# Optimization experiments

Measured on AMD Instinct MI355X. Metric: run time of the kernel, lower is better.

## Reference

```python
import jax, jax.numpy as jnp
import numpy as np

ALPHA = 0.5  # trapezoidal_alpha

def rmsnorm(x, w, eps=1e-5):
    return x * jax.lax.rsqrt(jnp.mean(x * x, axis=-1, keepdims=True) + eps) * w

def ssd_scan(x, Bc, Cc, dt, A, alpha):
    # x: (B,L,H,P), Bc/Cc: (B,L,N), dt: (B,L,H), A: (H,)
    da = jnp.exp(dt * A)  # (B,L,H), A < 0 so da in (0,1)
    shift = lambda t: jnp.concatenate([jnp.zeros_like(t[:, :1]), t[:, :-1]], axis=1)
    xp, bp, dtp = shift(x), shift(Bc), shift(dt)
    to_t = lambda t: jnp.moveaxis(t, 1, 0)
    xs = tuple(map(to_t, (x, Bc, Cc, dt, da, xp, bp, dtp)))
    Bb, _, H, P = x.shape
    N = Bc.shape[-1]
    h0 = jnp.zeros((Bb, H, P, N), x.dtype)
    def step(h, inp):
        xt, bt, ct, dtt, dat, xpt, bpt, dtpt = inp
        u = dtt[:, :, None, None] * xt[..., None] * bt[:, None, None, :]      # (B,H,P,N)
        up = dtpt[:, :, None, None] * xpt[..., None] * bpt[:, None, None, :]  # prev input term
        h = dat[:, :, None, None] * (h + alpha * up) + (1.0 - alpha) * u      # trapezoidal update
        y = jnp.einsum('bhpn,bn->bhp', h, ct)
        return h, y
    _, ys = jax.lax.scan(step, h0, xs)
    return jnp.moveaxis(ys, 0, 1)  # (B,L,H,P)

def setup_inputs() -> dict:
    key = jax.random.key(0)
    ks = jax.random.split(key, 10)
    B, NV, NQ = 4, 256, 32
    D, DI, H, N, E, NL = 1024, 2048, 32, 128, 1536, 12
    PROJ = 2 * DI + 2 * N + H  # z | x | B | C | dt
    s = 0.02
    return {
        'visual_tokens': jax.random.normal(ks[0], (B, NV, D), jnp.float32),
        'query_embeds': jax.random.normal(ks[1], (B, NQ, D), jnp.float32),
        'vis_w': jax.random.normal(ks[2], (D, D), jnp.float32) * s,
        'vis_b': jnp.zeros((D,), jnp.float32),
        'qry_w': jax.random.normal(ks[3], (D, D), jnp.float32) * s,
        'qry_b': jnp.zeros((D,), jnp.float32),
        'norm_ws': jnp.ones((NL, D), jnp.float32),
        'in_ws': jax.random.normal(ks[4], (NL, D, PROJ), jnp.float32) * s,
        'dt_biases': jax.random.normal(ks[5], (NL, H), jnp.float32) * 0.5,
        'A_logs': jnp.log(jnp.tile(jnp.arange(1.0, H + 1.0, dtype=jnp.float32)[None], (NL, 1))),
        'D_ssm': jnp.ones((NL, H), jnp.float32),
        'gnorm_ws': jnp.ones((NL, DI), jnp.float32),
        'out_ws': jax.random.normal(ks[6], (NL, DI, D), jnp.float32) * s,
        'norm_f_w': jnp.ones((D,), jnp.float32),
        'head_w': jax.random.normal(ks[7], (D, E), jnp.float32) * s,
        'head_b': jnp.zeros((E,), jnp.float32),
    }

def reference(visual_tokens, query_embeds, vis_w, vis_b, qry_w, qry_b, norm_ws, in_ws,
              dt_biases, A_logs, D_ssm, gnorm_ws, out_ws, norm_f_w, head_w, head_b):
    vis = visual_tokens @ vis_w + vis_b
    qry = query_embeds @ qry_w + qry_b
    hidden = jnp.concatenate([vis, qry], axis=1)  # (B,L,D)
    n_layers = in_ws.shape[0]
    d_inner = gnorm_ws.shape[-1]
    H = A_logs.shape[-1]
    P = d_inner // H
    N = (in_ws.shape[-1] - 2 * d_inner - H) // 2
    for i in range(n_layers):
        res = hidden
        xin = rmsnorm(hidden, norm_ws[i])
        proj = xin @ in_ws[i]  # (B,L,2*DI+2*N+H)
        z = proj[..., :d_inner]
        xss = proj[..., d_inner:2 * d_inner]
        Bc = proj[..., 2 * d_inner:2 * d_inner + N]
        Cc = proj[..., 2 * d_inner + N:2 * d_inner + 2 * N]
        dt = jax.nn.softplus(proj[..., 2 * d_inner + 2 * N:] + dt_biases[i])
        A = -jnp.exp(A_logs[i])
        xr = xss.reshape(xss.shape[0], xss.shape[1], H, P)
        y = ssd_scan(xr, Bc, Cc, dt, A, ALPHA) + D_ssm[i][None, None, :, None] * xr
        y = y.reshape(xss.shape)
        y = rmsnorm(y * jax.nn.silu(z), gnorm_ws[i])  # gated RMSNorm
        hidden = res + y @ out_ws[i]
    hidden = rmsnorm(hidden, norm_f_w)
    pooled = hidden.mean(axis=1)                   # (B,D)
    out = pooled @ head_w + head_b                 # (B,E)
    nrm = jnp.linalg.norm(out, axis=-1, keepdims=True)
    return out / jnp.maximum(nrm, 1e-12)           # F.normalize semantics
```

## Files before the change

kernel.cpp:

```cpp
#include <hip/hip_runtime.h>
#include <cmath>

#define Bb   4
#define Tt   288
#define Dd   1024
#define DIi  2048
#define HH   32
#define PP   64
#define NNs  128
#define PROJ  4384
#define PROJP 4480
#define NLl  12
#define EE   1536

typedef __bf16 bf16x8 __attribute__((ext_vector_type(8)));
typedef float f32x4 __attribute__((ext_vector_type(4)));
typedef float f32x16 __attribute__((ext_vector_type(16)));

__device__ __forceinline__ unsigned short f2bf(float v) {
  __bf16 b = (__bf16)v;
  return __builtin_bit_cast(unsigned short, b);
}
__device__ __forceinline__ float bf2f(unsigned short u) {
  unsigned int x = ((unsigned int)u) << 16;
  return __builtin_bit_cast(float, x);
}
__device__ __forceinline__ void split2(float v, unsigned short& h, unsigned short& l) {
  h = f2bf(v);
  l = f2bf(v - bf2f(h));
}

__device__ __forceinline__ size_t packed_off(int row, int k, int K) {
  size_t tile = (size_t)(row >> 5) * (K >> 5) + (k >> 5);
  int half = (k >> 4) & 1;
  int lane = (row & 31) + (((k >> 3) & 1) << 5);
  return tile * 1024 + half * 512 + lane * 8 + (k & 7);
}

__device__ __forceinline__ void async16(const void* g, void* l) {
  __builtin_amdgcn_global_load_lds(
      (const __attribute__((address_space(1))) unsigned int*)g,
      (__attribute__((address_space(3))) unsigned int*)l, 16, 0, 0);
}

__device__ inline float block_reduce_sum(float v, float* lds) {
#pragma unroll
  for (int d = 32; d > 0; d >>= 1) v += __shfl_down(v, d, 64);
  int lane = threadIdx.x & 63;
  int w = threadIdx.x >> 6;
  if (lane == 0) lds[w] = v;
  __syncthreads();
  if (threadIdx.x == 0) {
    float s = lds[0];
    int nw = blockDim.x >> 6;
    for (int i = 1; i < nw; i++) s += lds[i];
    lds[0] = s;
  }
  __syncthreads();
  return lds[0];
}

__global__ __launch_bounds__(256) void cvt_act_k(const float* __restrict__ vis,
                                                 const float* __restrict__ qry,
                                                 unsigned short* __restrict__ oh,
                                                 unsigned short* __restrict__ ol) {
  int idx = (blockIdx.x * 256 + threadIdx.x) * 4;
  const float* src = (idx < 1024 * 1024) ? &vis[idx] : &qry[idx - 1024 * 1024];
  float4 v = *(const float4*)src;
  ushort4 h, l;
  split2(v.x, h.x, l.x); split2(v.y, h.y, l.y);
  split2(v.z, h.z, l.z); split2(v.w, h.w, l.w);
  size_t po = packed_off(idx >> 10, idx & 1023, 1024);
  *(ushort4*)&oh[po] = h;
  *(ushort4*)&ol[po] = l;
}

__global__ __launch_bounds__(256) void cvt_tr2_k(const float* __restrict__ W,
                                                 unsigned short* __restrict__ Wth,
                                                 unsigned short* __restrict__ Wtl,
                                                 int K, int N,
                                                 size_t wstride, size_t ostride) {
  __shared__ float tile[32][33];
  W   += (size_t)blockIdx.z * wstride;
  Wth += (size_t)blockIdx.z * ostride;
  Wtl += (size_t)blockIdx.z * ostride;
  const int n0 = blockIdx.x * 32, k0 = blockIdx.y * 32;
  const int c = threadIdx.x & 31;
  const int r0 = threadIdx.x >> 5;
#pragma unroll
  for (int j = 0; j < 4; j++) {
    int r = r0 + j * 8;
    int n = n0 + c;
    tile[r][c] = (n < N) ? W[(size_t)(k0 + r) * N + n] : 0.f;
  }
  __syncthreads();
  const int nl = threadIdx.x >> 3;
  const int kl = (threadIdx.x & 7) * 4;
  ushort4 h, l;
  split2(tile[kl + 0][nl], h.x, l.x);
  split2(tile[kl + 1][nl], h.y, l.y);
  split2(tile[kl + 2][nl], h.z, l.z);
  split2(tile[kl + 3][nl], h.w, l.w);
  size_t o = packed_off(n0 + nl, k0 + kl, K);
  *(ushort4*)&Wth[o] = h;
  *(ushort4*)&Wtl[o] = l;
}

template<int BM, int BN>
__global__ __launch_bounds__(256) void gemm3_k(
    const unsigned short* __restrict__ Ah, const unsigned short* __restrict__ Al,
    const unsigned short* __restrict__ Wh, const unsigned short* __restrict__ Wl,
    const float* __restrict__ bias, const float* __restrict__ res,
    float* __restrict__ C, int M, int N, int K,
    int rows_per_b, int T_total, int t_off)
{
  constexpr int FM = BM / 64;
  constexpr int FN = BN / 64;
  __shared__ __align__(16) unsigned short Ash[BM * 32];
  __shared__ __align__(16) unsigned short Asl[BM * 32];
  __shared__ __align__(16) unsigned short Bsh[BN * 32];
  __shared__ __align__(16) unsigned short Bsl[BN * 32];
  const int tid = threadIdx.x;
  const int lane = tid & 63;
  const int wm = (tid >> 6) >> 1;
  const int wn = (tid >> 6) & 1;
  const int m0 = blockIdx.y * BM;
  const int n0 = blockIdx.x * BN;
  const int lrow = lane & 31;
  const int kb32 = K >> 5;

  f32x16 acc[FM][FN];
#pragma unroll
  for (int i = 0; i < FM; i++)
#pragma unroll
    for (int j = 0; j < FN; j++) acc[i][j] = (f32x16)0.0f;

  for (int kb = 0; kb < kb32; kb++) {
#pragma unroll
    for (int c = 0; c < BM / 64; c++) {
      int o = (c * 256 + tid) * 16;
      int t = o >> 11;
      size_t gb = (((size_t)((m0 >> 5) + t) * kb32 + kb) << 11) + (o & 2047);
      async16((const char*)Ah + gb, (char*)Ash + o);
      async16((const char*)Al + gb, (char*)Asl + o);
    }
#pragma unroll
    for (int c = 0; c < BN / 64; c++) {
      int o = (c * 256 + tid) * 16;
      int t = o >> 11;
      size_t gb = (((size_t)((n0 >> 5) + t) * kb32 + kb) << 11) + (o & 2047);
      async16((const char*)Wh + gb, (char*)Bsh + o);
      async16((const char*)Wl + gb, (char*)Bsl + o);
    }
    __syncthreads();

#pragma unroll
    for (int kh = 0; kh < 2; kh++) {
      bf16x8 ah[FM], al[FM], bh[FN], bl[FN];
#pragma unroll
      for (int i = 0; i < FM; i++) {
        int off = (wm * FM + i) * 1024 + kh * 512 + lane * 8;
        ah[i] = *(const bf16x8*)&Ash[off];
        al[i] = *(const bf16x8*)&Asl[off];
      }
#pragma unroll
      for (int j = 0; j < FN; j++) {
        int off = (wn * FN + j) * 1024 + kh * 512 + lane * 8;
        bh[j] = *(const bf16x8*)&Bsh[off];
        bl[j] = *(const bf16x8*)&Bsl[off];
      }
#pragma unroll
      for (int i = 0; i < FM; i++)
#pragma unroll
        for (int j = 0; j < FN; j++) {
          acc[i][j] = __builtin_amdgcn_mfma_f32_32x32x16_bf16(ah[i], bh[j], acc[i][j], 0, 0, 0);
          acc[i][j] = __builtin_amdgcn_mfma_f32_32x32x16_bf16(ah[i], bl[j], acc[i][j], 0, 0, 0);
          acc[i][j] = __builtin_amdgcn_mfma_f32_32x32x16_bf16(al[i], bh[j], acc[i][j], 0, 0, 0);
        }
    }
    __syncthreads();
  }

  const int r0 = (lane >> 5) * 4;
#pragma unroll
  for (int i = 0; i < FM; i++) {
#pragma unroll
    for (int j = 0; j < FN; j++) {
      int ncol = n0 + wn * (BN / 2) + j * 32 + lrow;
      float bv = bias ? bias[ncol] : 0.f;
#pragma unroll
      for (int rg = 0; rg < 16; rg++) {
        int m = m0 + wm * (BM / 2) + i * 32 + (rg & 3) + 8 * (rg >> 2) + r0;
        size_t orow;
        if (T_total) {
          int bbv = m / rows_per_b;
          orow = (size_t)bbv * T_total + (m - bbv * rows_per_b) + t_off;
        } else {
          orow = (size_t)m;
        }
        float v = acc[i][j][rg] + bv;
        if (res) v += res[orow * N + ncol];
        C[orow * N + ncol] = v;
      }
    }
  }
}

__global__ __launch_bounds__(256) void gemm_k(
    const float* __restrict__ A, const float* __restrict__ W,
    const float* __restrict__ bias, const float* __restrict__ res,
    float* __restrict__ C, int M, int N, int K,
    int rows_per_b, int T_total, int t_off)
{
  __shared__ float As[16][64];
  __shared__ float Ws[16][64];
  const int tid = threadIdx.x;
  const int tx = tid & 15;
  const int ty = tid >> 4;
  const int m0 = blockIdx.y * 64;
  const int n0 = blockIdx.x * 64;
  float acc[4][4] = {};
  const int ar = tid >> 2;
  const int ac = (tid & 3) << 2;
  const int wr = tid >> 4;
  const int wc = (tid & 15) << 2;

  for (int k0 = 0; k0 < K; k0 += 16) {
    float4 av = {0.f, 0.f, 0.f, 0.f};
    int gr = m0 + ar;
    if (gr < M) av = *(const float4*)&A[(size_t)gr * K + k0 + ac];
    As[ac + 0][ar] = av.x; As[ac + 1][ar] = av.y;
    As[ac + 2][ar] = av.z; As[ac + 3][ar] = av.w;

    float4 wv = {0.f, 0.f, 0.f, 0.f};
    int gc = n0 + wc;
    const float* wp = &W[(size_t)(k0 + wr) * N + gc];
    if (gc + 3 < N) {
      wv = *(const float4*)wp;
    } else {
      if (gc + 0 < N) wv.x = wp[0];
      if (gc + 1 < N) wv.y = wp[1];
      if (gc + 2 < N) wv.z = wp[2];
    }
    *(float4*)&Ws[wr][wc] = wv;
    __syncthreads();
#pragma unroll
    for (int kk = 0; kk < 16; kk++) {
      float4 a4 = *(const float4*)&As[kk][ty << 2];
      float4 b4 = *(const float4*)&Ws[kk][tx << 2];
      float a[4] = {a4.x, a4.y, a4.z, a4.w};
      float b[4] = {b4.x, b4.y, b4.z, b4.w};
#pragma unroll
      for (int i = 0; i < 4; i++)
#pragma unroll
        for (int j = 0; j < 4; j++)
          acc[i][j] = fmaf(a[i], b[j], acc[i][j]);
    }
    __syncthreads();
  }
#pragma unroll
  for (int i = 0; i < 4; i++) {
    int gr = m0 + (ty << 2) + i;
    if (gr >= M) continue;
    int bbv = gr / rows_per_b;
    int tt = gr - bbv * rows_per_b;
    size_t orow = (size_t)bbv * T_total + tt + t_off;
#pragma unroll
    for (int j = 0; j < 4; j++) {
      int gc = n0 + (tx << 2) + j;
      if (gc >= N) continue;
      float v = acc[i][j];
      if (bias) v += bias[gc];
      if (res)  v += res[orow * (size_t)N + gc];
      C[orow * (size_t)N + gc] = v;
    }
  }
}

__global__ __launch_bounds__(256) void rmsnorm_k(
    const float* __restrict__ x, const float* __restrict__ w, float* __restrict__ out)
{
  __shared__ float lds[8];
  const int row = blockIdx.x;
  const float* xr = x + (size_t)row * Dd;
  float4 v = *(const float4*)&xr[threadIdx.x << 2];
  float ss = v.x * v.x + v.y * v.y + v.z * v.z + v.w * v.w;
  ss = block_reduce_sum(ss, lds);
  float sc = rsqrtf(ss * (1.f / Dd) + 1e-5f);
  float4 wv = *(const float4*)&w[threadIdx.x << 2];
  float4 o = {v.x * sc * wv.x, v.y * sc * wv.y, v.z * sc * wv.z, v.w * sc * wv.w};
  *(float4*)&out[(size_t)row * Dd + (threadIdx.x << 2)] = o;
}

__global__ __launch_bounds__(256) void rmsnorm2_k(
    const float* __restrict__ x, const float* __restrict__ w,
    unsigned short* __restrict__ oh, unsigned short* __restrict__ ol)
{
  __shared__ float lds[8];
  const int row = blockIdx.x;
  const float* xr = x + (size_t)row * Dd;
  float4 v = *(const float4*)&xr[threadIdx.x << 2];
  float ss = v.x * v.x + v.y * v.y + v.z * v.z + v.w * v.w;
  ss = block_reduce_sum(ss, lds);
  float sc = rsqrtf(ss * (1.f / Dd) + 1e-5f);
  float4 wv = *(const float4*)&w[threadIdx.x << 2];
  ushort4 h, l;
  split2(v.x * sc * wv.x, h.x, l.x);
  split2(v.y * sc * wv.y, h.y, l.y);
  split2(v.z * sc * wv.z, h.z, l.z);
  split2(v.w * sc * wv.w, h.w, l.w);
  size_t o = packed_off(row, threadIdx.x << 2, 1024);
  *(ushort4*)&oh[o] = h;
  *(ushort4*)&ol[o] = l;
}

__global__ __launch_bounds__(64) void dtcum_k(
    const float* __restrict__ proj, const float* __restrict__ dt_bias,
    const float* __restrict__ A_log,
    float* __restrict__ dtt, double* __restrict__ dcum)
{
  const int h = blockIdx.x & 31;
  const int b = blockIdx.x >> 5;
  const int lane = threadIdx.x;
  const float A = -expf(A_log[h]);
  const float bias = dt_bias[h];
  const int rowo = (b * HH + h) * Tt;
  double base = 0.0;
  for (int c = 0; c < (Tt + 63) / 64; c++) {
    int t = c * 64 + lane;
    float dt = 0.f;
    if (t < Tt) {
      float v = proj[(size_t)(b * Tt + t) * PROJP + 2 * DIi + 2 * NNs + h] + bias;
      dt = (v > 20.f) ? v : log1pf(expf(v));
    }
    double a = (double)(dt * A);
#pragma unroll
    for (int d = 1; d < 64; d <<= 1) {
      double o = __shfl_up(a, d, 64);
      if (lane >= d) a += o;
    }
    double cum = base + a;
    if (t < Tt) { dtt[rowo + t] = dt; dcum[rowo + t] = cum; }
    base = __shfl(cum, 63, 64);
  }
}

__global__ __launch_bounds__(256) void cbgemm_k(const float* __restrict__ proj,
                                                float* __restrict__ St)
{
  const int tI = blockIdx.x, jI = blockIdx.y, b = blockIdx.z;
  if (jI > tI) return;
  __shared__ float Ct[32][130];
  __shared__ float Bt[32][130];
  const int tid = threadIdx.x;
  const int r = tid >> 3;
  const int q = (tid & 7) * 16;
  const float* pb = proj + (size_t)b * Tt * PROJP;
  {
    const float* crow = pb + (size_t)(tI * 32 + r) * PROJP + 2 * DIi + NNs + q;
    const float* brow = pb + (size_t)(jI * 32 + r) * PROJP + 2 * DIi + q;
#pragma unroll
    for (int f = 0; f < 16; f += 4) {
      float4 c4 = *(const float4*)&crow[f];
      float4 b4 = *(const float4*)&brow[f];
      *(float2*)&Ct[r][q + f]     = make_float2(c4.x, c4.y);
      *(float2*)&Ct[r][q + f + 2] = make_float2(c4.z, c4.w);
      *(float2*)&Bt[r][q + f]     = make_float2(b4.x, b4.y);
      *(float2*)&Bt[r][q + f + 2] = make_float2(b4.z, b4.w);
    }
  }
  __syncthreads();
  const int j_r = tid >> 3;
  const int t_c = (tid & 7) * 4;
  float acc[4] = {0.f, 0.f, 0.f, 0.f};
  for (int n = 0; n < NNs; n += 2) {
    float2 b2 = *(const float2*)&Bt[j_r][n];
#pragma unroll
    for (int k = 0; k < 4; k++) {
      float2 c2 = *(const float2*)&Ct[t_c + k][n];
      acc[k] = fmaf(b2.x, c2.x, acc[k]);
      acc[k] = fmaf(b2.y, c2.y, acc[k]);
    }
  }
  float* so = St + ((size_t)b * Tt + jI * 32 + j_r) * Tt + tI * 32 + t_c;
  *(float4*)so = make_float4(acc[0], acc[1], acc[2], acc[3]);
}

__global__ __launch_bounds__(256) void ssd_y_k(
    const float* __restrict__ proj, const float* __restrict__ St,
    const float* __restrict__ dtt, const double* __restrict__ dcum,
    const float* __restrict__ Dssm, float* __restrict__ ybuf)
{
  const int tI = blockIdx.x;
  const int h  = blockIdx.y;
  const int b  = blockIdx.z;
  __shared__ __align__(16) float Xs[32][64];
  __shared__ __align__(16) float Ss[32][36];
  __shared__ double cjs[32];
  const int tid = threadIdx.x;
  const int t_l = tid & 31;
  const int pg  = tid >> 5;
  const int t0  = tI * 32;
  const int rowo = (b * HH + h) * Tt;
  const double ct = dcum[rowo + t0 + t_l];
  const float Ds = Dssm[h];
  const float* pb = proj + (size_t)b * Tt * PROJP;
  float y[8] = {0,0,0,0,0,0,0,0};
  const int sr = tid >> 3;
  const int sq = tid & 7;

  for (int jI = 0; jI <= tI; jI++) {
    const int j0 = jI * 32;
    {
      const float* xr = pb + (size_t)(j0 + sr) * PROJP + DIi + h * PP + sq * 8;
      *(float4*)&Xs[sr][sq * 8]     = *(const float4*)&xr[0];
      *(float4*)&Xs[sr][sq * 8 + 4] = *(const float4*)&xr[4];
    }
    {
      const float* srow = St + ((size_t)b * Tt + j0 + sr) * Tt + t0 + sq * 4;
      float4 s4 = *(const float4*)srow;
      float dj = dtt[rowo + j0 + sr];
      s4.x *= dj; s4.y *= dj; s4.z *= dj; s4.w *= dj;
      *(float4*)&Ss[sr][sq * 4] = s4;
    }
    if (tid < 32) cjs[tid] = dcum[rowo + j0 + tid];
    __syncthreads();

    if (jI < tI) {
#pragma unroll 4
      for (int j = 0; j < 32; j++) {
        float d = (float)(ct - cjs[j]);
        float m = Ss[j][t_l] * expf(fminf(d, 0.f));
        const float* xp = &Xs[j][pg * 8];
        float4 a0 = *(const float4*)&xp[0];
        float4 a1 = *(const float4*)&xp[4];
        y[0] = fmaf(m, a0.x, y[0]); y[1] = fmaf(m, a0.y, y[1]);
        y[2] = fmaf(m, a0.z, y[2]); y[3] = fmaf(m, a0.w, y[3]);
        y[4] = fmaf(m, a1.x, y[4]); y[5] = fmaf(m, a1.y, y[5]);
        y[6] = fmaf(m, a1.z, y[6]); y[7] = fmaf(m, a1.w, y[7]);
      }
    } else {
      for (int j = 0; j < 32; j++) {
        float sv = Ss[j][t_l];
        float d = (float)(ct - cjs[j]);
        float m = sv * expf(fminf(d, 0.f));
        if (j == t_l) m = 0.5f * sv + Ds;
        if (j > t_l)  m = 0.f;
        const float* xp = &Xs[j][pg * 8];
        float4 a0 = *(const float4*)&xp[0];
        float4 a1 = *(const float4*)&xp[4];
        y[0] = fmaf(m, a0.x, y[0]); y[1] = fmaf(m, a0.y, y[1]);
        y[2] = fmaf(m, a0.z, y[2]); y[3] = fmaf(m, a0.w, y[3]);
        y[4] = fmaf(m, a1.x, y[4]); y[5] = fmaf(m, a1.y, y[5]);
        y[6] = fmaf(m, a1.z, y[6]); y[7] = fmaf(m, a1.w, y[7]);
      }
    }
    __syncthreads();
  }
  float* yo = &ybuf[(size_t)(b * Tt + t0 + t_l) * DIi + h * PP + pg * 8];
  *(float4*)&yo[0] = make_float4(y[0], y[1], y[2], y[3]);
  *(float4*)&yo[4] = make_float4(y[4], y[5], y[6], y[7]);
}

__global__ __launch_bounds__(256) void gate_norm2_k(
    const float* __restrict__ ybuf, const float* __restrict__ proj,
    const float* __restrict__ gw,
    unsigned short* __restrict__ yh, unsigned short* __restrict__ yl)
{
  __shared__ float lds[8];
  const int row = blockIdx.x;
  const float* yr = ybuf + (size_t)row * DIi;
  const float* zr = proj + (size_t)row * PROJP;
  const int base = threadIdx.x << 3;
  float4 z0 = *(const float4*)&zr[base];
  float4 z1 = *(const float4*)&zr[base + 4];
  float4 y0 = *(const float4*)&yr[base];
  float4 y1 = *(const float4*)&yr[base + 4];
  float zz[8] = {z0.x, z0.y, z0.z, z0.w, z1.x, z1.y, z1.z, z1.w};
  float yy[8] = {y0.x, y0.y, y0.z, y0.w, y1.x, y1.y, y1.z, y1.w};
  float g[8];
  float ss = 0.f;
#pragma unroll
  for (int e = 0; e < 8; e++) {
    float s = zz[e] / (1.f + expf(-zz[e]));
    float gv = yy[e] * s;
    g[e] = gv;
    ss += gv * gv;
  }
  ss = block_reduce_sum(ss, lds);
  float sc = rsqrtf(ss * (1.f / DIi) + 1e-5f);
  ushort4 h0, l0, h1, l1;
  split2(g[0] * sc * gw[base + 0], h0.x, l0.x);
  split2(g[1] * sc * gw[base + 1], h0.y, l0.y);
  split2(g[2] * sc * gw[base + 2], h0.z, l0.z);
  split2(g[3] * sc * gw[base + 3], h0.w, l0.w);
  split2(g[4] * sc * gw[base + 4], h1.x, l1.x);
  split2(g[5] * sc * gw[base + 5], h1.y, l1.y);
  split2(g[6] * sc * gw[base + 6], h1.z, l1.z);
  split2(g[7] * sc * gw[base + 7], h1.w, l1.w);
  size_t o = packed_off(row, base, 2048);
  *(ushort4*)&yh[o] = h0; *(ushort4*)&yh[o + 4] = h1;
  *(ushort4*)&yl[o] = l0; *(ushort4*)&yl[o + 4] = l1;
}

__global__ void pool_k(const float* __restrict__ xin, float* __restrict__ pooled) {
  int b = blockIdx.x;
  int d = blockIdx.y * 256 + threadIdx.x;
  const float* base = xin + (size_t)b * Tt * Dd + d;
  float s = 0.f;
  for (int t = 0; t < Tt; t++) s += base[(size_t)t * Dd];
  pooled[b * Dd + d] = s * (1.f / Tt);
}

__global__ __launch_bounds__(256) void l2norm_k(float* __restrict__ out) {
  __shared__ float lds[8];
  const int row = blockIdx.x;
  float* r = out + (size_t)row * EE;
  float v[6];
  float ss = 0.f;
#pragma unroll
  for (int e = 0; e < 6; e++) {
    v[e] = r[(e << 8) + threadIdx.x];
    ss += v[e] * v[e];
  }
  ss = block_reduce_sum(ss, lds);
  float sc = 1.f / fmaxf(sqrtf(ss), 1e-12f);
#pragma unroll
  for (int e = 0; e < 6; e++) r[(e << 8) + threadIdx.x] = v[e] * sc;
}

extern "C" void kernel_launch(void* const* d_in, const int* in_sizes, int n_in,
                              void* d_out, int out_size, void* d_ws, size_t ws_size,
                              hipStream_t stream) {
  (void)in_sizes; (void)n_in; (void)out_size;
  const float* visual   = (const float*)d_in[0];
  const float* query    = (const float*)d_in[1];
  const float* vis_w    = (const float*)d_in[2];
  const float* vis_b    = (const float*)d_in[3];
  const float* qry_w    = (const float*)d_in[4];
  const float* qry_b    = (const float*)d_in[5];
  const float* norm_ws  = (const float*)d_in[6];
  const float* in_ws    = (const float*)d_in[7];
  const float* dt_biases= (const float*)d_in[8];
  const float* A_logs   = (const float*)d_in[9];
  const float* D_ssm    = (const float*)d_in[10];
  const float* gnorm_ws = (const float*)d_in[11];
  const float* out_ws   = (const float*)d_in[12];
  const float* norm_f_w = (const float*)d_in[13];
  const float* head_w   = (const float*)d_in[14];
  const float* head_b   = (const float*)d_in[15];
  float* out = (float*)d_out;

  char* w = (char*)d_ws;
  float*          hidden = (float*)w;          w += (size_t)1152 * 1024 * 4;
  unsigned short* xh     = (unsigned short*)w; w += (size_t)1152 * 1024 * 2;
  unsigned short* xl     = (unsigned short*)w; w += (size_t)1152 * 1024 * 2;
  float*          proj   = (float*)w;          w += (size_t)1152 * PROJP * 4;
  float*          ybuf   = (float*)w;          w += (size_t)1152 * 2048 * 4;
  unsigned short* yh     = (unsigned short*)w; w += (size_t)1152 * 2048 * 2;
  unsigned short* yl     = (unsigned short*)w; w += (size_t)1152 * 2048 * 2;
  float*          dtt    = (float*)w;          w += (size_t)Bb * HH * Tt * 4;
  double*         dcum   = (double*)w;         w += (size_t)Bb * HH * Tt * 8;
  float*          Stb    = (float*)w;          w += (size_t)Bb * Tt * Tt * 4;
  float*          pooled = (float*)w;          w += (size_t)4096 * 4;
  unsigned short* wth    = (unsigned short*)w; w += (size_t)PROJP * 1024 * 2;
  unsigned short* wtl    = (unsigned short*)w; w += (size_t)PROJP * 1024 * 2;

  unsigned short* wtin_h  = (unsigned short*)w; w += (size_t)NLl * PROJP * 1024 * 2;
  unsigned short* wtin_l  = (unsigned short*)w; w += (size_t)NLl * PROJP * 1024 * 2;
  unsigned short* wtout_h = (unsigned short*)w; w += (size_t)NLl * 1024 * 2048 * 2;
  unsigned short* wtout_l = (unsigned short*)w; w += (size_t)NLl * 1024 * 2048 * 2;
  unsigned short* wtv_h   = (unsigned short*)w; w += (size_t)1024 * 1024 * 2;
  unsigned short* wtv_l   = (unsigned short*)w; w += (size_t)1024 * 1024 * 2;
  unsigned short* wtq_h   = (unsigned short*)w; w += (size_t)1024 * 1024 * 2;
  unsigned short* wtq_l   = (unsigned short*)w; w += (size_t)1024 * 1024 * 2;
  const bool batched = ((size_t)(w - (char*)d_ws)) <= ws_size;

  dim3 blk(256);

  cvt_act_k<<<1152, blk, 0, stream>>>(visual, query, xh, xl);

  if (batched) {
    cvt_tr2_k<<<dim3(32, 32, 1), blk, 0, stream>>>(vis_w, wtv_h, wtv_l, 1024, 1024, 0, 0);
    cvt_tr2_k<<<dim3(32, 32, 1), blk, 0, stream>>>(qry_w, wtq_h, wtq_l, 1024, 1024, 0, 0);
    cvt_tr2_k<<<dim3(PROJP / 32, 32, NLl), blk, 0, stream>>>(
        in_ws, wtin_h, wtin_l, Dd, PROJ, (size_t)Dd * PROJ, (size_t)PROJP * 1024);
    cvt_tr2_k<<<dim3(32, 64, NLl), blk, 0, stream>>>(
        out_ws, wtout_h, wtout_l, DIi, Dd, (size_t)DIi * Dd, (size_t)1024 * 2048);
    gemm3_k<64, 64><<<dim3(16, 16), blk, 0, stream>>>(
        xh, xl, wtv_h, wtv_l, vis_b, nullptr, hidden, 1024, 1024, 1024, 256, Tt, 0);
    gemm3_k<64, 64><<<dim3(16, 2), blk, 0, stream>>>(
        xh + (size_t)1024 * 1024, xl + (size_t)1024 * 1024, wtq_h, wtq_l,
        qry_b, nullptr, hidden, 128, 1024, 1024, 32, Tt, 256);
  } else {
    cvt_tr2_k<<<dim3(32, 32, 1), blk, 0, stream>>>(vis_w, wth, wtl, 1024, 1024, 0, 0);
    gemm3_k<64, 64><<<dim3(16, 16), blk, 0, stream>>>(
        xh, xl, wth, wtl, vis_b, nullptr, hidden, 1024, 1024, 1024, 256, Tt, 0);
    cvt_tr2_k<<<dim3(32, 32, 1), blk, 0, stream>>>(qry_w, wth, wtl, 1024, 1024, 0, 0);
    gemm3_k<64, 64><<<dim3(16, 2), blk, 0, stream>>>(
        xh + (size_t)1024 * 1024, xl + (size_t)1024 * 1024, wth, wtl,
        qry_b, nullptr, hidden, 128, 1024, 1024, 32, Tt, 256);
  }

  for (int i = 0; i < NLl; i++) {
    rmsnorm2_k<<<Bb * Tt, blk, 0, stream>>>(hidden, norm_ws + i * Dd, xh, xl);
    const unsigned short *bih, *bil;
    if (batched) {
      bih = wtin_h + (size_t)i * PROJP * 1024;
      bil = wtin_l + (size_t)i * PROJP * 1024;
    } else {
      cvt_tr2_k<<<dim3(PROJP / 32, 32, 1), blk, 0, stream>>>(
          in_ws + (size_t)i * Dd * PROJ, wth, wtl, Dd, PROJ, 0, 0);
      bih = wth; bil = wtl;
    }
    gemm3_k<128, 128><<<dim3(PROJP / 128, 9), blk, 0, stream>>>(
        xh, xl, bih, bil, nullptr, nullptr, proj, 1152, PROJP, Dd, 1152, 0, 0);
    dtcum_k<<<Bb * HH, dim3(64), 0, stream>>>(proj, dt_biases + i * HH,
                                              A_logs + i * HH, dtt, dcum);
    cbgemm_k<<<dim3(9, 9, Bb), blk, 0, stream>>>(proj, Stb);
    ssd_y_k<<<dim3(9, HH, Bb), blk, 0, stream>>>(proj, Stb, dtt, dcum,
                                                 D_ssm + i * HH, ybuf);
    gate_norm2_k<<<Bb * Tt, blk, 0, stream>>>(ybuf, proj, gnorm_ws + i * DIi, yh, yl);
    const unsigned short *boh, *bol;
    if (batched) {
      boh = wtout_h + (size_t)i * 1024 * 2048;
      bol = wtout_l + (size_t)i * 1024 * 2048;
    } else {
      cvt_tr2_k<<<dim3(32, 64, 1), blk, 0, stream>>>(
          out_ws + (size_t)i * DIi * Dd, wth, wtl, DIi, Dd, 0, 0);
      boh = wth; bol = wtl;
    }
    gemm3_k<64, 64><<<dim3(16, 18), blk, 0, stream>>>(
        yh, yl, boh, bol, nullptr, hidden, hidden, 1152, Dd, DIi, 1152, 0, 0);
  }

  rmsnorm_k<<<Bb * Tt, blk, 0, stream>>>(hidden, norm_f_w, ybuf);
  pool_k<<<dim3(Bb, 4), blk, 0, stream>>>(ybuf, pooled);
  gemm_k<<<dim3(24, 1), blk, 0, stream>>>(pooled, head_w, head_b, nullptr, out,
                                          Bb, EE, Dd, Bb, 0, 0);
  l2norm_k<<<Bb, blk, 0, stream>>>(out);
}
```

Before: 2.930 ms.

## Double-buffer GEMM B tiles, load A to registers, fuse dt-cumsum with CB gemm

```diff
diff --git a/kernel.cpp b/kernel.cpp
--- a/kernel.cpp
+++ b/kernel.cpp
@@ -64,15 +64,18 @@
                                                  const float* __restrict__ qry,
                                                  unsigned short* __restrict__ oh,
                                                  unsigned short* __restrict__ ol) {
-  int idx = (blockIdx.x * 256 + threadIdx.x) * 4;
+  int idx = (blockIdx.x * 256 + threadIdx.x) * 8;
   const float* src = (idx < 1024 * 1024) ? &vis[idx] : &qry[idx - 1024 * 1024];
-  float4 v = *(const float4*)src;
-  ushort4 h, l;
-  split2(v.x, h.x, l.x); split2(v.y, h.y, l.y);
-  split2(v.z, h.z, l.z); split2(v.w, h.w, l.w);
+  float4 v0 = *(const float4*)&src[0];
+  float4 v1 = *(const float4*)&src[4];
+  ushort4 h0, l0, h1, l1;
+  split2(v0.x, h0.x, l0.x); split2(v0.y, h0.y, l0.y);
+  split2(v0.z, h0.z, l0.z); split2(v0.w, h0.w, l0.w);
+  split2(v1.x, h1.x, l1.x); split2(v1.y, h1.y, l1.y);
+  split2(v1.z, h1.z, l1.z); split2(v1.w, h1.w, l1.w);
   size_t po = packed_off(idx >> 10, idx & 1023, 1024);
-  *(ushort4*)&oh[po] = h;
-  *(ushort4*)&ol[po] = l;
+  *(ushort4*)&oh[po] = h0; *(ushort4*)&oh[po + 4] = h1;
+  *(ushort4*)&ol[po] = l0; *(ushort4*)&ol[po + 4] = l1;
 }
 
 __global__ __launch_bounds__(256) void cvt_tr2_k(const float* __restrict__ W,
@@ -80,30 +83,30 @@
                                                  unsigned short* __restrict__ Wtl,
                                                  int K, int N,
                                                  size_t wstride, size_t ostride) {
-  __shared__ float tile[32][33];
+  __shared__ float tile[64][33];
   W   += (size_t)blockIdx.z * wstride;
   Wth += (size_t)blockIdx.z * ostride;
   Wtl += (size_t)blockIdx.z * ostride;
-  const int n0 = blockIdx.x * 32, k0 = blockIdx.y * 32;
+  const int n0 = blockIdx.x * 32, k0 = blockIdx.y * 64;
   const int c = threadIdx.x & 31;
   const int r0 = threadIdx.x >> 5;
 #pragma unroll
-  for (int j = 0; j < 4; j++) {
+  for (int j = 0; j < 8; j++) {
     int r = r0 + j * 8;
     int n = n0 + c;
     tile[r][c] = (n < N) ? W[(size_t)(k0 + r) * N + n] : 0.f;
   }
   __syncthreads();
-  const int nl = threadIdx.x >> 3;
-  const int kl = (threadIdx.x & 7) * 4;
-  ushort4 h, l;
-  split2(tile[kl + 0][nl], h.x, l.x);
-  split2(tile[kl + 1][nl], h.y, l.y);
-  split2(tile[kl + 2][nl], h.z, l.z);
-  split2(tile[kl + 3][nl], h.w, l.w);
-  size_t o = packed_off(n0 + nl, k0 + kl, K);
-  *(ushort4*)&Wth[o] = h;
-  *(ushort4*)&Wtl[o] = l;
+  const int nl = threadIdx.x & 31;
+  const int kg = threadIdx.x >> 5;
+  unsigned short h[8], l[8];
+#pragma unroll
+  for (int j = 0; j < 8; j++) split2(tile[kg * 8 + j][nl], h[j], l[j]);
+  size_t o = packed_off(n0 + nl, k0 + kg * 8, K);
+  *(ushort4*)&Wth[o]     = make_ushort4(h[0], h[1], h[2], h[3]);
+  *(ushort4*)&Wth[o + 4] = make_ushort4(h[4], h[5], h[6], h[7]);
+  *(ushort4*)&Wtl[o]     = make_ushort4(l[0], l[1], l[2], l[3]);
+  *(ushort4*)&Wtl[o + 4] = make_ushort4(l[4], l[5], l[6], l[7]);
 }
 
 template<int BM, int BN>
@@ -116,10 +119,10 @@
 {
   constexpr int FM = BM / 64;
   constexpr int FN = BN / 64;
-  __shared__ __align__(16) unsigned short Ash[BM * 32];
-  __shared__ __align__(16) unsigned short Asl[BM * 32];
-  __shared__ __align__(16) unsigned short Bsh[BN * 32];
-  __shared__ __align__(16) unsigned short Bsl[BN * 32];
+  __shared__ __align__(16) unsigned short Bsh0[BN * 32];
+  __shared__ __align__(16) unsigned short Bsl0[BN * 32];
+  __shared__ __align__(16) unsigned short Bsh1[BN * 32];
+  __shared__ __align__(16) unsigned short Bsl1[BN * 32];
   const int tid = threadIdx.x;
   const int lane = tid & 63;
   const int wm = (tid >> 6) >> 1;
@@ -135,49 +138,60 @@
 #pragma unroll
     for (int j = 0; j < FN; j++) acc[i][j] = (f32x16)0.0f;
 
-  for (int kb = 0; kb < kb32; kb++) {
-#pragma unroll
-    for (int c = 0; c < BM / 64; c++) {
-      int o = (c * 256 + tid) * 16;
-      int t = o >> 11;
-      size_t gb = (((size_t)((m0 >> 5) + t) * kb32 + kb) << 11) + (o & 2047);
-      async16((const char*)Ah + gb, (char*)Ash + o);
-      async16((const char*)Al + gb, (char*)Asl + o);
-    }
+  auto stageB = [&](unsigned short* dH, unsigned short* dL, int kb) {
 #pragma unroll
     for (int c = 0; c < BN / 64; c++) {
       int o = (c * 256 + tid) * 16;
       int t = o >> 11;
       size_t gb = (((size_t)((n0 >> 5) + t) * kb32 + kb) << 11) + (o & 2047);
-      async16((const char*)Wh + gb, (char*)Bsh + o);
-      async16((const char*)Wl + gb, (char*)Bsl + o);
-    }
-    __syncthreads();
-
+      async16((const char*)Wh + gb, (char*)dH + o);
+      async16((const char*)Wl + gb, (char*)dL + o);
+    }
+  };
+  bf16x8 a0h[FM][2], a0l[FM][2], a1h[FM][2], a1l[FM][2];
+  auto loadA = [&](bf16x8 (&rh)[FM][2], bf16x8 (&rl)[FM][2], int kb) {
+#pragma unroll
+    for (int i = 0; i < FM; i++)
+#pragma unroll
+      for (int kh = 0; kh < 2; kh++) {
+        size_t ga = ((size_t)((m0 >> 5) + wm * FM + i) * kb32 + kb) * 1024
+                  + kh * 512 + (size_t)lane * 8;
+        rh[i][kh] = *(const bf16x8*)&Ah[ga];
+        rl[i][kh] = *(const bf16x8*)&Al[ga];
+      }
+  };
+  auto compute = [&](bf16x8 (&rh)[FM][2], bf16x8 (&rl)[FM][2],
+                     const unsigned short* BH, const unsigned short* BL) {
 #pragma unroll
     for (int kh = 0; kh < 2; kh++) {
-      bf16x8 ah[FM], al[FM], bh[FN], bl[FN];
-#pragma unroll
-      for (int i = 0; i < FM; i++) {
-        int off = (wm * FM + i) * 1024 + kh * 512 + lane * 8;
-        ah[i] = *(const bf16x8*)&Ash[off];
-        al[i] = *(const bf16x8*)&Asl[off];
-      }
+      bf16x8 bh[FN], bl[FN];
 #pragma unroll
       for (int j = 0; j < FN; j++) {
         int off = (wn * FN + j) * 1024 + kh * 512 + lane * 8;
-        bh[j] = *(const bf16x8*)&Bsh[off];
-        bl[j] = *(const bf16x8*)&Bsl[off];
+        bh[j] = *(const bf16x8*)&BH[off];
+        bl[j] = *(const bf16x8*)&BL[off];
       }
 #pragma unroll
       for (int i = 0; i < FM; i++)
 #pragma unroll
         for (int j = 0; j < FN; j++) {
-          acc[i][j] = __builtin_amdgcn_mfma_f32_32x32x16_bf16(ah[i], bh[j], acc[i][j], 0, 0, 0);
-          acc[i][j] = __builtin_amdgcn_mfma_f32_32x32x16_bf16(ah[i], bl[j], acc[i][j], 0, 0, 0);
-          acc[i][j] = __builtin_amdgcn_mfma_f32_32x32x16_bf16(al[i], bh[j], acc[i][j], 0, 0, 0);
+          acc[i][j] = __builtin_amdgcn_mfma_f32_32x32x16_bf16(rh[i][kh], bh[j], acc[i][j], 0, 0, 0);
+          acc[i][j] = __builtin_amdgcn_mfma_f32_32x32x16_bf16(rh[i][kh], bl[j], acc[i][j], 0, 0, 0);
+          acc[i][j] = __builtin_amdgcn_mfma_f32_32x32x16_bf16(rl[i][kh], bh[j], acc[i][j], 0, 0, 0);
         }
     }
+  };
+
+  stageB(Bsh0, Bsl0, 0);
+  loadA(a0h, a0l, 0);
+  __syncthreads();
+  for (int kb = 0; kb < kb32; kb += 2) {
+    stageB(Bsh1, Bsl1, kb + 1);
+    loadA(a1h, a1l, kb + 1);
+    compute(a0h, a0l, Bsh0, Bsl0);
+    __syncthreads();
+    if (kb + 2 < kb32) { stageB(Bsh0, Bsl0, kb + 2); loadA(a0h, a0l, kb + 2); }
+    compute(a1h, a1l, Bsh1, Bsl1);
     __syncthreads();
   }
 
@@ -314,44 +328,46 @@
   *(ushort4*)&ol[o] = l;
 }
 
-__global__ __launch_bounds__(64) void dtcum_k(
-    const float* __restrict__ proj, const float* __restrict__ dt_bias,
-    const float* __restrict__ A_log,
-    float* __restrict__ dtt, double* __restrict__ dcum)
+__global__ __launch_bounds__(256) void sscb_k(const float* __restrict__ proj,
+                                              const float* __restrict__ dt_bias,
+                                              const float* __restrict__ A_log,
+                                              float* __restrict__ dtt,
+                                              double* __restrict__ dcum,
+                                              float* __restrict__ St)
 {
-  const int h = blockIdx.x & 31;
-  const int b = blockIdx.x >> 5;
-  const int lane = threadIdx.x;
-  const float A = -expf(A_log[h]);
-  const float bias = dt_bias[h];
-  const int rowo = (b * HH + h) * Tt;
-  double base = 0.0;
-  for (int c = 0; c < (Tt + 63) / 64; c++) {
-    int t = c * 64 + lane;
-    float dt = 0.f;
-    if (t < Tt) {
-      float v = proj[(size_t)(b * Tt + t) * PROJP + 2 * DIi + 2 * NNs + h] + bias;
-      dt = (v > 20.f) ? v : log1pf(expf(v));
-    }
-    double a = (double)(dt * A);
-#pragma unroll
-    for (int d = 1; d < 64; d <<= 1) {
-      double o = __shfl_up(a, d, 64);
-      if (lane >= d) a += o;
-    }
-    double cum = base + a;
-    if (t < Tt) { dtt[rowo + t] = dt; dcum[rowo + t] = cum; }
-    base = __shfl(cum, 63, 64);
-  }
-}
-
-__global__ __launch_bounds__(256) void cbgemm_k(const float* __restrict__ proj,
-                                                float* __restrict__ St)
-{
+  __shared__ float Ct[32][130];
+  __shared__ float Bt[32][130];
+  if (blockIdx.y == 9) {
+    if (blockIdx.x >= 8) return;
+    const int wv = threadIdx.x >> 6;
+    const int lane = threadIdx.x & 63;
+    const int h = blockIdx.x * 4 + wv;
+    const int b = blockIdx.z;
+    const float A = -expf(A_log[h]);
+    const float bias = dt_bias[h];
+    const int rowo = (b * HH + h) * Tt;
+    double base = 0.0;
+    for (int c = 0; c < (Tt + 63) / 64; c++) {
+      int t = c * 64 + lane;
+      float dt = 0.f;
+      if (t < Tt) {
+        float v = proj[(size_t)(b * Tt + t) * PROJP + 2 * DIi + 2 * NNs + h] + bias;
+        dt = (v > 20.f) ? v : log1pf(expf(v));
+      }
+      double a = (double)(dt * A);
+#pragma unroll
+      for (int d = 1; d < 64; d <<= 1) {
+        double o = __shfl_up(a, d, 64);
+        if (lane >= d) a += o;
+      }
+      double cum = base + a;
+      if (t < Tt) { dtt[rowo + t] = dt; dcum[rowo + t] = cum; }
+      base = __shfl(cum, 63, 64);
+    }
+    return;
+  }
   const int tI = blockIdx.x, jI = blockIdx.y, b = blockIdx.z;
   if (jI > tI) return;
-  __shared__ float Ct[32][130];
-  __shared__ float Bt[32][130];
   const int tid = threadIdx.x;
   const int r = tid >> 3;
   const int q = (tid & 7) * 16;
@@ -578,26 +594,26 @@
 
   dim3 blk(256);
 
-  cvt_act_k<<<1152, blk, 0, stream>>>(visual, query, xh, xl);
+  cvt_act_k<<<576, blk, 0, stream>>>(visual, query, xh, xl);
 
   if (batched) {
-    cvt_tr2_k<<<dim3(32, 32, 1), blk, 0, stream>>>(vis_w, wtv_h, wtv_l, 1024, 1024, 0, 0);
-    cvt_tr2_k<<<dim3(32, 32, 1), blk, 0, stream>>>(qry_w, wtq_h, wtq_l, 1024, 1024, 0, 0);
-    cvt_tr2_k<<<dim3(PROJP / 32, 32, NLl), blk, 0, stream>>>(
+    cvt_tr2_k<<<dim3(32, 16, 1), blk, 0, stream>>>(vis_w, wtv_h, wtv_l, 1024, 1024, 0, 0);
+    cvt_tr2_k<<<dim3(32, 16, 1), blk, 0, stream>>>(qry_w, wtq_h, wtq_l, 1024, 1024, 0, 0);
+    cvt_tr2_k<<<dim3(PROJP / 32, 16, NLl), blk, 0, stream>>>(
         in_ws, wtin_h, wtin_l, Dd, PROJ, (size_t)Dd * PROJ, (size_t)PROJP * 1024);
-    cvt_tr2_k<<<dim3(32, 64, NLl), blk, 0, stream>>>(
+    cvt_tr2_k<<<dim3(32, 32, NLl), blk, 0, stream>>>(
         out_ws, wtout_h, wtout_l, DIi, Dd, (size_t)DIi * Dd, (size_t)1024 * 2048);
-    gemm3_k<64, 64><<<dim3(16, 16), blk, 0, stream>>>(
+    gemm3_k<128, 64><<<dim3(16, 8), blk, 0, stream>>>(
         xh, xl, wtv_h, wtv_l, vis_b, nullptr, hidden, 1024, 1024, 1024, 256, Tt, 0);
-    gemm3_k<64, 64><<<dim3(16, 2), blk, 0, stream>>>(
+    gemm3_k<128, 64><<<dim3(16, 1), blk, 0, stream>>>(
         xh + (size_t)1024 * 1024, xl + (size_t)1024 * 1024, wtq_h, wtq_l,
         qry_b, nullptr, hidden, 128, 1024, 1024, 32, Tt, 256);
   } else {
-    cvt_tr2_k<<<dim3(32, 32, 1), blk, 0, stream>>>(vis_w, wth, wtl, 1024, 1024, 0, 0);
-    gemm3_k<64, 64><<<dim3(16, 16), blk, 0, stream>>>(
+    cvt_tr2_k<<<dim3(32, 16, 1), blk, 0, stream>>>(vis_w, wth, wtl, 1024, 1024, 0, 0);
+    gemm3_k<128, 64><<<dim3(16, 8), blk, 0, stream>>>(
         xh, xl, wth, wtl, vis_b, nullptr, hidden, 1024, 1024, 1024, 256, Tt, 0);
-    cvt_tr2_k<<<dim3(32, 32, 1), blk, 0, stream>>>(qry_w, wth, wtl, 1024, 1024, 0, 0);
-    gemm3_k<64, 64><<<dim3(16, 2), blk, 0, stream>>>(
+    cvt_tr2_k<<<dim3(32, 16, 1), blk, 0, stream>>>(qry_w, wth, wtl, 1024, 1024, 0, 0);
+    gemm3_k<128, 64><<<dim3(16, 1), blk, 0, stream>>>(
         xh + (size_t)1024 * 1024, xl + (size_t)1024 * 1024, wth, wtl,
         qry_b, nullptr, hidden, 128, 1024, 1024, 32, Tt, 256);
   }
@@ -609,15 +625,14 @@
       bih = wtin_h + (size_t)i * PROJP * 1024;
       bil = wtin_l + (size_t)i * PROJP * 1024;
     } else {
-      cvt_tr2_k<<<dim3(PROJP / 32, 32, 1), blk, 0, stream>>>(
+      cvt_tr2_k<<<dim3(PROJP / 32, 16, 1), blk, 0, stream>>>(
           in_ws + (size_t)i * Dd * PROJ, wth, wtl, Dd, PROJ, 0, 0);
       bih = wth; bil = wtl;
     }
     gemm3_k<128, 128><<<dim3(PROJP / 128, 9), blk, 0, stream>>>(
         xh, xl, bih, bil, nullptr, nullptr, proj, 1152, PROJP, Dd, 1152, 0, 0);
-    dtcum_k<<<Bb * HH, dim3(64), 0, stream>>>(proj, dt_biases + i * HH,
-                                              A_logs + i * HH, dtt, dcum);
-    cbgemm_k<<<dim3(9, 9, Bb), blk, 0, stream>>>(proj, Stb);
+    sscb_k<<<dim3(9, 10, Bb), blk, 0, stream>>>(proj, dt_biases + i * HH,
+                                                A_logs + i * HH, dtt, dcum, Stb);
     ssd_y_k<<<dim3(9, HH, Bb), blk, 0, stream>>>(proj, Stb, dtt, dcum,
                                                  D_ssm + i * HH, ybuf);
     gate_norm2_k<<<Bb * Tt, blk, 0, stream>>>(ybuf, proj, gnorm_ws + i * DIi, yh, yl);
@@ -626,11 +641,11 @@
       boh = wtout_h + (size_t)i * 1024 * 2048;
       bol = wtout_l + (size_t)i * 1024 * 2048;
     } else {
-      cvt_tr2_k<<<dim3(32, 64, 1), blk, 0, stream>>>(
+      cvt_tr2_k<<<dim3(32, 32, 1), blk, 0, stream>>>(
           out_ws + (size_t)i * DIi * Dd, wth, wtl, DIi, Dd, 0, 0);
       boh = wth; bol = wtl;
     }
-    gemm3_k<64, 64><<<dim3(16, 18), blk, 0, stream>>>(
+    gemm3_k<128, 64><<<dim3(16, 9), blk, 0, stream>>>(
         yh, yl, boh, bol, nullptr, hidden, hidden, 1152, Dd, DIi, 1152, 0, 0);
   }
 
```

New measurement: 3.114 ms. +6.3%, slower.
